# Performance work log

Hardware: AMD Instinct MI355X
Metric: run time of the kernel (lower is better)

The kernel has to match this reference:

```python
import jax, jax.numpy as jnp
import numpy as np

EMBED = 192
EXPAND = 3
D1 = EMBED * EXPAND  # 576
RPE_IN = 32
LAYERS = 3
LAMBDA = 0.95


def _rpe_mlp(t, w0, b0, ws, bs, wo, bo):
    # t: (2n, 1) relative positions -> (2n, D1) Toeplitz coefficients
    h = t @ w0.T + b0
    for i in range(ws.shape[0]):
        h = jax.nn.relu(h) @ ws[i].T + bs[i]
    return jax.nn.relu(h) @ wo.T + bo


def _toeplitz(x, a):
    # Toeplitz matmul via length-2n circular convolution (FFT).
    # x: (B, n, d); a: (2n, d) coeffs ordered [t0, t1..t_{n-1}, pad, neg half]
    n = x.shape[1]
    m = 2 * n
    xf = jnp.fft.rfft(x, m, axis=1)
    af = jnp.fft.rfft(a, m, axis=0)
    return jnp.fft.irfft(xf * af[None], m, axis=1)[:, :n]


def _forward(x, p_w, p_b, q_w, q_b, v_w, v_b, o_w, o_b, slope,
             t1_w0, t1_b0, t1_ws, t1_bs, t1_wo, t1_bo,
             t2_w0, t2_b0, t2_ws, t2_bs, t2_wo, t2_bo):
    b, h, w, d = x.shape
    n = h  # square grid: h == w, rpe/decay built from n = x.shape[1]
    dt = x.dtype

    pos = jnp.arange(1, n, dtype=dt).reshape(-1, 1)          # (n-1, 1)
    zero = jnp.zeros((1, 1), dt)
    rpe_input = jnp.concatenate([zero, pos, zero, -pos], axis=0)  # (2n, 1)

    p = jax.nn.silu(x @ p_w.T + p_b)
    q = jax.nn.silu(x @ q_w.T + q_b)
    v = jax.nn.silu(x @ v_w.T + v_b)

    # decay mask: slope clamped to [0,1], blended with lambda, powered by |lag|
    sl = LAMBDA + (1.0 - LAMBDA) * jnp.clip(slope, 0.0, 1.0)  # (1, D1)
    idx = jnp.arange(1, n, dtype=dt).reshape(1, -1, 1)        # (1, n-1, 1)
    gamma = sl ** idx                                          # (1, n-1, D1)
    one = jnp.ones((1, 1, D1), dt)
    decay = jnp.concatenate([one, gamma, one, gamma[:, ::-1]], axis=1)[0]  # (2n, D1)

    a1 = _rpe_mlp(rpe_input, t1_w0, t1_b0, t1_ws, t1_bs, t1_wo, t1_bo) * decay
    a2 = _rpe_mlp(rpe_input, t2_w0, t2_b0, t2_ws, t2_bs, t2_wo, t2_bo) * decay

    qv = q * v                                                 # (b, h, w, D1)
    # axial mixing: tno1 along width, tno2 along height
    o1 = _toeplitz(qv.reshape(b * h, w, D1), a1).reshape(b, h, w, D1)
    o2 = _toeplitz(jnp.transpose(qv, (0, 2, 1, 3)).reshape(b * w, h, D1), a2)
    o2 = jnp.transpose(o2.reshape(b, w, h, D1), (0, 2, 1, 3))
    out = p * (o1 + o2)
    return out @ o_w.T + o_b


def setup_inputs() -> dict:
    key = jax.random.key(0)
    ks = jax.random.split(key, 8)

    def lin(k, out_d, in_d):
        k1, k2 = jax.random.split(k)
        s = 1.0 / np.sqrt(in_d)
        return (jax.random.uniform(k1, (out_d, in_d), jnp.float32, -s, s),
                jax.random.uniform(k2, (out_d,), jnp.float32, -s, s))

    x = jax.random.normal(ks[0], (8, 56, 56, EMBED), jnp.float32)
    p_w, p_b = lin(ks[1], D1, EMBED)
    q_w, q_b = lin(ks[2], D1, EMBED)
    v_w, v_b = lin(ks[3], D1, EMBED)
    o_w, o_b = lin(ks[4], EMBED, D1)
    # slope init: 1/arange(1, d1+1)^(1/(index+1)), index=0
    slope = (1.0 / jnp.arange(1, D1 + 1, dtype=jnp.float32)).reshape(1, -1)

    def tno_params(kb):
        kk = jax.random.split(kb, 2 + LAYERS)
        w0, b0 = lin(kk[0], RPE_IN, 1)
        ws, bs = [], []
        for i in range(LAYERS):
            wi, bi = lin(kk[1 + i], RPE_IN, RPE_IN)
            ws.append(wi); bs.append(bi)
        wo, bo = lin(kk[1 + LAYERS], D1, RPE_IN)
        return w0, b0, jnp.stack(ws), jnp.stack(bs), wo, bo

    t1 = tno_params(ks[5])
    t2 = tno_params(ks[6])
    return {"x": x, "p_w": p_w, "p_b": p_b, "q_w": q_w, "q_b": q_b,
            "v_w": v_w, "v_b": v_b, "o_w": o_w, "o_b": o_b, "slope": slope,
            "t1_w0": t1[0], "t1_b0": t1[1], "t1_ws": t1[2], "t1_bs": t1[3], "t1_wo": t1[4], "t1_bo": t1[5],
            "t2_w0": t2[0], "t2_b0": t2[1], "t2_ws": t2[2], "t2_bs": t2[3], "t2_wo": t2[4], "t2_bo": t2[5]}


def reference(x, p_w, p_b, q_w, q_b, v_w, v_b, o_w, o_b, slope,
              t1_w0, t1_b0, t1_ws, t1_bs, t1_wo, t1_bo,
              t2_w0, t2_b0, t2_ws, t2_bs, t2_wo, t2_bo):
    return _forward(x, p_w, p_b, q_w, q_b, v_w, v_b, o_w, o_b, slope,
                    t1_w0, t1_b0, t1_ws, t1_bs, t1_wo, t1_bo,
                    t2_w0, t2_b0, t2_ws, t2_bs, t2_wo, t2_bo)
```

## Files before the change

### kernel.cpp

```cpp
#include <hip/hip_runtime.h>
#include <hip/hip_bf16.h>
#include <math.h>

typedef unsigned short u16;
typedef short bf16x8 __attribute__((ext_vector_type(8)));
typedef float f32x4 __attribute__((ext_vector_type(4)));

#define NB 8
#define NN 56
#define M2 112
#define EMB 192
#define D1 576
#define TOK (NB*NN*NN)

__device__ __forceinline__ float bf2f(unsigned int u) {
    union { unsigned int i; float f; } v; v.i = u << 16; return v.f;
}
__device__ __forceinline__ u16 f2bf(float f) {
    union { float f; unsigned int i; } v; v.f = f;
    unsigned int x = v.i;
    return (u16)((x + 0x7fffu + ((x >> 16) & 1u)) >> 16);
}
__device__ __forceinline__ float fast_silu(float x) {
    float e = __builtin_amdgcn_exp2f(-1.442695041f * x);
    return x * __builtin_amdgcn_rcpf(1.0f + e);
}
__device__ __forceinline__ void async16(void* lds, const void* g) {
    __builtin_amdgcn_global_load_lds(
        (const __attribute__((address_space(1))) void*)g,
        (__attribute__((address_space(3))) void*)lds, 16, 0, 0);
}

#define XCH (TOK*EMB/4)
#define WCH (D1*EMB/4)
__global__ __launch_bounds__(256) void convert_kernel(
    const float* __restrict__ x,
    const float* __restrict__ pw, const float* __restrict__ qw,
    const float* __restrict__ vw, const float* __restrict__ ow,
    u16* __restrict__ xb, u16* __restrict__ wb, u16* __restrict__ owb)
{
    int tid = blockIdx.x * 256 + threadIdx.x;
    const float* src; u16* dst; int off;
    if (tid < XCH) { src = x; dst = xb; off = tid; }
    else {
        int r = tid - XCH;
        int seg = r / WCH; off = r % WCH;
        if (seg == 0)      { src = pw; dst = wb; }
        else if (seg == 1) { src = qw; dst = wb + D1*EMB; }
        else if (seg == 2) { src = vw; dst = wb + 2*D1*EMB; }
        else if (seg == 3) { src = ow; dst = owb; }
        else return;
    }
    float4 f = *(const float4*)(src + off * 4);
    ushort4 o;
    o.x = f2bf(f.x); o.y = f2bf(f.y); o.z = f2bf(f.z); o.w = f2bf(f.w);
    *(ushort4*)(dst + off * 4) = o;
}

__global__ __launch_bounds__(576) void rpe_kernel(
    const float* __restrict__ slope,
    const float* w0a, const float* b0a, const float* wsa, const float* bsa,
    const float* woa, const float* boa,
    const float* w0b, const float* b0b, const float* wsb, const float* bsb,
    const float* wob, const float* bob,
    float* __restrict__ A1, float* __restrict__ A2)
{
    int wq  = blockIdx.x / M2;
    int row = blockIdx.x % M2;
    const float* w0 = wq ? w0b : w0a;  const float* b0 = wq ? b0b : b0a;
    const float* ws = wq ? wsb : wsa;  const float* bs = wq ? bsb : bsa;
    const float* wo = wq ? wob : woa;  const float* bo = wq ? bob : boa;
    float* A = wq ? A2 : A1;

    float tval = (row == 0 || row == 56) ? 0.0f
               : (row < 56 ? (float)row : -(float)(row - 56));
    int kexp = (row == 0 || row == 56) ? 0 : (row < 56 ? row : 112 - row);

    __shared__ float h[32], g[32];
    int t = threadIdx.x;
    if (t < 32) h[t] = tval * w0[t] + b0[t];
    __syncthreads();
    for (int L = 0; L < 3; L++) {
        if (t < 32) g[t] = fmaxf(h[t], 0.0f);
        __syncthreads();
        float hn = 0.0f;
        if (t < 32) {
            hn = bs[L * 32 + t];
            for (int k = 0; k < 32; k++)
                hn = fmaf(g[k], ws[(L * 32 + t) * 32 + k], hn);
        }
        __syncthreads();
        if (t < 32) h[t] = hn;
        __syncthreads();
    }
    if (t < 32) g[t] = fmaxf(h[t], 0.0f);
    __syncthreads();

    float o = bo[t];
    for (int k = 0; k < 32; k++)
        o = fmaf(g[k], wo[t * 32 + k], o);

    float sl = slope[t];
    sl = 0.95f + 0.05f * fminf(fmaxf(sl, 0.0f), 1.0f);
    float dec = powf(sl, (float)kexp);
    A[row * D1 + t] = o * dec;
}

__global__ __launch_bounds__(256) void tbuild_kernel(
    const float* __restrict__ A1, const float* __restrict__ A2,
    u16* __restrict__ T1t, u16* __restrict__ T2t)
{
    int d = blockIdx.x;
    const float* src = blockIdx.y ? A2 : A1;
    u16* dst = blockIdx.y ? T2t : T1t;
    __shared__ float win[111];
    int t = threadIdx.x;
    if (t < 111) {
        int lag = t - 55;
        int rowi = lag + (lag < 0 ? 112 : 0);
        win[t] = src[rowi * D1 + d];
    }
    __syncthreads();
    int i = t >> 2, jq = (t & 3) * 16;
    u16 vals[16];
    #pragma unroll
    for (int jj = 0; jj < 16; jj++) {
        int j = jq + jj;
        float v = (i < 56 && j < 56) ? win[i - j + 55] : 0.0f;
        vals[jj] = f2bf(v);
    }
    u16* out = dst + ((size_t)d * 64 + i) * 64 + jq;
    *(uint4*)(out)     = *(uint4*)&vals[0];
    *(uint4*)(out + 8) = *(uint4*)&vals[8];
}

__global__ __launch_bounds__(512, 4) void proj_kernel(
    const u16* __restrict__ xb, const u16* __restrict__ wb,
    const float* __restrict__ pb, const float* __restrict__ qb,
    const float* __restrict__ vb,
    u16* __restrict__ P_T, u16* __restrict__ QV_T)
{
    __shared__ u16 lds[20480];
    int m0 = blockIdx.x * 128, n0 = blockIdx.y * 64;
    int t = threadIdx.x;
    int l = t & 63, wave = t >> 6;
    int wm = wave >> 2, wn = wave & 3;
    int col16 = l & 15, q = l >> 4;

    f32x4 accp[4], accq[4], accv[4];
    #pragma unroll
    for (int i = 0; i < 4; i++) {
        accp[i] = (f32x4){0,0,0,0};
        accq[i] = (f32x4){0,0,0,0};
        accv[i] = (f32x4){0,0,0,0};
    }

    auto stage = [&](int kc) {
        #pragma unroll
        for (int ii = 0; ii < 2; ii++) {
            int slot = ii * 512 + t;
            int r = slot >> 3, s = slot & 7;
            int g = s ^ (r & 7);
            async16(&lds[slot * 8], xb + (m0 + r) * EMB + kc * 64 + g * 8);
        }
        #pragma unroll
        for (int ii = 0; ii < 3; ii++) {
            int slot = ii * 512 + t;
            int mat = slot >> 9, cc = slot & 511;
            int r = cc >> 3, s = cc & 7;
            int g = s ^ (r & 7);
            async16(&lds[8192 + slot * 8],
                    wb + mat * (D1 * EMB) + (n0 + r) * EMB + kc * 64 + g * 8);
        }
    };

    #pragma unroll
    for (int kc = 0; kc < 3; kc++) {
        stage(kc);
        asm volatile("s_waitcnt vmcnt(0)" ::: "memory");
        __builtin_amdgcn_s_barrier();
        #pragma unroll
        for (int kk = 0; kk < 2; kk++) {
            int sw = ((q + 4 * kk) ^ (col16 & 7)) * 8;
            bf16x8 af[4];
            #pragma unroll
            for (int mt = 0; mt < 4; mt++)
                af[mt] = *(const bf16x8*)&lds[(wm * 64 + mt * 16 + col16) * 64 + sw];
            bf16x8 bfr[3];
            #pragma unroll
            for (int mat = 0; mat < 3; mat++)
                bfr[mat] = *(const bf16x8*)&lds[8192 + mat * 4096 + (wn * 16 + col16) * 64 + sw];
            #pragma unroll
            for (int mt = 0; mt < 4; mt++) {
                accp[mt] = __builtin_amdgcn_mfma_f32_16x16x32_bf16(af[mt], bfr[0], accp[mt], 0, 0, 0);
                accq[mt] = __builtin_amdgcn_mfma_f32_16x16x32_bf16(af[mt], bfr[1], accq[mt], 0, 0, 0);
                accv[mt] = __builtin_amdgcn_mfma_f32_16x16x32_bf16(af[mt], bfr[2], accv[mt], 0, 0, 0);
            }
        }
        if (kc < 2) __builtin_amdgcn_s_barrier();
    }

    int n = n0 + wn * 16 + col16;
    float pbv = pb[n], qbv = qb[n], vbv = vb[n];
    size_t drow = (size_t)n * TOK + m0 + wm * 64;
    #pragma unroll
    for (int mt = 0; mt < 4; mt++) {
        ushort4 o;
        o.x = f2bf(fast_silu(accp[mt][0] + pbv));
        o.y = f2bf(fast_silu(accp[mt][1] + pbv));
        o.z = f2bf(fast_silu(accp[mt][2] + pbv));
        o.w = f2bf(fast_silu(accp[mt][3] + pbv));
        *(ushort4*)&P_T[drow + mt * 16 + q * 4] = o;
    }
    #pragma unroll
    for (int mt = 0; mt < 4; mt++) {
        ushort4 o;
        o.x = f2bf(fast_silu(accq[mt][0] + qbv) * fast_silu(accv[mt][0] + vbv));
        o.y = f2bf(fast_silu(accq[mt][1] + qbv) * fast_silu(accv[mt][1] + vbv));
        o.z = f2bf(fast_silu(accq[mt][2] + qbv) * fast_silu(accv[mt][2] + vbv));
        o.w = f2bf(fast_silu(accq[mt][3] + qbv) * fast_silu(accv[mt][3] + vbv));
        *(ushort4*)&QV_T[drow + mt * 16 + q * 4] = o;
    }
}

__global__ __launch_bounds__(256) void tno_mfma(
    const u16* __restrict__ QV_T, const u16* __restrict__ T1t,
    const u16* __restrict__ T2t, const u16* __restrict__ P_T,
    u16* __restrict__ U_T)
{
    __shared__ u16 T1s[4096];
    __shared__ u16 T2s[4096];
    __shared__ u16 Qn[64 * 72];
    __shared__ u16 Qt[64 * 72];
    __shared__ float O1f[56 * 68];
    int d = blockIdx.x, b = blockIdx.y;
    int t = threadIdx.x;
    size_t base = (size_t)d * TOK + (size_t)b * 3136;

    #pragma unroll
    for (int k = 0; k < 2; k++) {
        int slot = t + k * 256;
        int i = slot >> 3, s = slot & 7;
        int g = s ^ (i & 7);
        async16(&T1s[slot * 8], T1t + ((size_t)d * 64 + i) * 64 + g * 8);
        async16(&T2s[slot * 8], T2t + ((size_t)d * 64 + i) * 64 + g * 8);
    }
    for (int c = t; c < 392; c += 256) {
        int h = c / 7, w8 = (c % 7) * 8;
        uint4 v = *(const uint4*)(QV_T + base + c * 8);
        *(uint4*)&Qn[h * 72 + w8] = v;
        u16 e[8];
        *(uint4*)e = v;
        #pragma unroll
        for (int k = 0; k < 8; k++)
            Qt[(w8 + k) * 72 + h] = e[k];
    }
    if (t < 56) {
        uint4 z = {0, 0, 0, 0};
        *(uint4*)&Qn[t * 72 + 56] = z;
        *(uint4*)&Qt[t * 72 + 56] = z;
    }
    __syncthreads();

    int l = t & 63, wave = t >> 6;
    int col16 = l & 15, q = l >> 4;

    f32x4 acc1[4], acc2[4];
    #pragma unroll
    for (int i = 0; i < 4; i++) { acc1[i] = (f32x4){0,0,0,0}; acc2[i] = (f32x4){0,0,0,0}; }

    #pragma unroll
    for (int kk = 0; kk < 2; kk++) {
        int sw = ((q + 4 * kk) ^ (col16 & 7)) * 8;
        bf16x8 bq1 = *(const bf16x8*)&Qn[(wave * 16 + col16) * 72 + kk * 32 + q * 8];
        bf16x8 bq2 = *(const bf16x8*)&Qt[(wave * 16 + col16) * 72 + kk * 32 + q * 8];
        #pragma unroll
        for (int mt = 0; mt < 4; mt++) {
            bf16x8 a1 = *(const bf16x8*)&T1s[(mt * 16 + col16) * 64 + sw];
            bf16x8 a2 = *(const bf16x8*)&T2s[(mt * 16 + col16) * 64 + sw];
            acc1[mt] = __builtin_amdgcn_mfma_f32_16x16x32_bf16(a1, bq1, acc1[mt], 0, 0, 0);
            acc2[mt] = __builtin_amdgcn_mfma_f32_16x16x32_bf16(a2, bq2, acc2[mt], 0, 0, 0);
        }
    }

    {
        int n = wave * 16 + col16;
        if (n < 56) {
            #pragma unroll
            for (int mt = 0; mt < 4; mt++)
                #pragma unroll
                for (int r = 0; r < 4; r++) {
                    int m = mt * 16 + q * 4 + r;
                    if (m < 56) O1f[n * 68 + m] = acc1[mt][r];
                }
        }
    }
    __syncthreads();
    {
        int n = wave * 16 + col16;
        if (n < 56) {
            #pragma unroll
            for (int mt = 0; mt < 4; mt++)
                #pragma unroll
                for (int r = 0; r < 4; r++) {
                    int m = mt * 16 + q * 4 + r;
                    if (m < 56) O1f[m * 68 + n] += acc2[mt][r];
                }
        }
    }
    __syncthreads();
    for (int c = t; c < 392; c += 256) {
        int h = c / 7, w8 = (c % 7) * 8;
        f32x4 s0 = *(const f32x4*)&O1f[h * 68 + w8];
        f32x4 s1 = *(const f32x4*)&O1f[h * 68 + w8 + 4];
        uint4 pv = *(const uint4*)(P_T + base + c * 8);
        u16 pe[8];
        *(uint4*)pe = pv;
        u16 ue[8];
        #pragma unroll
        for (int k = 0; k < 4; k++) ue[k] = f2bf(bf2f(pe[k]) * s0[k]);
        #pragma unroll
        for (int k = 0; k < 4; k++) ue[4 + k] = f2bf(bf2f(pe[4 + k]) * s1[k]);
        *(uint4*)(U_T + base + c * 8) = *(uint4*)ue;
    }
}

__global__ __launch_bounds__(256) void outproj_kernel(
    const u16* __restrict__ U_T, const u16* __restrict__ owb,
    const float* __restrict__ ob, float* __restrict__ out)
{
    __shared__ char ldsraw[40960];
    u16* Uscr = (u16*)ldsraw;
    u16* As   = (u16*)(ldsraw + 16384);
    u16* Bs   = (u16*)(ldsraw + 32768);
    int m0 = blockIdx.x * 128, n0 = blockIdx.y * 64;
    int t = threadIdx.x;
    int l = t & 63, wave = t >> 6;
    int wm = wave >> 1, wn = wave & 1;
    int col16 = l & 15, q = l >> 4;

    f32x4 acc[4][2];
    #pragma unroll
    for (int i = 0; i < 4; i++)
        #pragma unroll
        for (int j = 0; j < 2; j++) acc[i][j] = (f32x4){0,0,0,0};

    for (int k0 = 0; k0 < 9; k0++) {
        #pragma unroll
        for (int ii = 0; ii < 4; ii++) {
            int slot = ii * 256 + t;
            int dd = slot >> 4, tk = slot & 15;
            async16(&Uscr[slot * 8],
                    U_T + (size_t)(k0 * 64 + dd) * TOK + m0 + tk * 8);
        }
        #pragma unroll
        for (int ii = 0; ii < 2; ii++) {
            int slot = ii * 256 + t;
            int r = slot >> 3, s = slot & 7;
            int g = s ^ (r & 7);
            async16(&Bs[slot * 8], owb + (n0 + r) * D1 + k0 * 64 + g * 8);
        }
        asm volatile("s_waitcnt vmcnt(2)" ::: "memory");
        __builtin_amdgcn_s_barrier();
        #pragma unroll
        for (int ii = 0; ii < 4; ii++) {
            int c = ii * 256 + t;
            int tok = c & 127, dc = c >> 7;
            u16 e[8];
            #pragma unroll
            for (int j = 0; j < 8; j++)
                e[j] = Uscr[(dc * 8 + j) * 128 + tok];
            int s = dc ^ (tok & 7);
            *(uint4*)&As[tok * 64 + s * 8] = *(uint4*)e;
        }
        __syncthreads();

        #pragma unroll
        for (int kk = 0; kk < 2; kk++) {
            int sw = ((q + 4 * kk) ^ (col16 & 7)) * 8;
            bf16x8 af[4];
            #pragma unroll
            for (int mt = 0; mt < 4; mt++)
                af[mt] = *(const bf16x8*)&As[(wm * 64 + mt * 16 + col16) * 64 + sw];
            bf16x8 bfr[2];
            #pragma unroll
            for (int nt = 0; nt < 2; nt++)
                bfr[nt] = *(const bf16x8*)&Bs[(wn * 32 + nt * 16 + col16) * 64 + sw];
            #pragma unroll
            for (int mt = 0; mt < 4; mt++)
                #pragma unroll
                for (int nt = 0; nt < 2; nt++)
                    acc[mt][nt] = __builtin_amdgcn_mfma_f32_16x16x32_bf16(
                        af[mt], bfr[nt], acc[mt][nt], 0, 0, 0);
        }
        __syncthreads();
    }

    float* scr = (float*)ldsraw + wave * 2304;
    float obv[2];
    #pragma unroll
    for (int nt = 0; nt < 2; nt++)
        obv[nt] = ob[n0 + wn * 32 + nt * 16 + col16];
    #pragma unroll
    for (int mt = 0; mt < 4; mt++)
        #pragma unroll
        for (int nt = 0; nt < 2; nt++)
            #pragma unroll
            for (int r = 0; r < 4; r++)
                scr[(mt * 16 + q * 4 + r) * 36 + nt * 16 + col16] =
                    acc[mt][nt][r] + obv[nt];
    __syncthreads();
    #pragma unroll
    for (int k = 0; k < 8; k++) {
        int row = k * 8 + (l >> 3), cs = (l & 7) * 4;
        f32x4 v = *(const f32x4*)&scr[row * 36 + cs];
        *(f32x4*)&out[(m0 + wm * 64 + row) * EMB + n0 + wn * 32 + cs] = v;
    }
}

extern "C" void kernel_launch(void* const* d_in, const int* in_sizes, int n_in,
                              void* d_out, int out_size, void* d_ws, size_t ws_size,
                              hipStream_t stream)
{
    (void)in_sizes; (void)n_in; (void)out_size; (void)ws_size;
    const float* x     = (const float*)d_in[0];
    const float* p_w   = (const float*)d_in[1];
    const float* p_b   = (const float*)d_in[2];
    const float* q_w   = (const float*)d_in[3];
    const float* q_b   = (const float*)d_in[4];
    const float* v_w   = (const float*)d_in[5];
    const float* v_b   = (const float*)d_in[6];
    const float* o_w   = (const float*)d_in[7];
    const float* o_b   = (const float*)d_in[8];
    const float* slope = (const float*)d_in[9];
    const float* t1_w0 = (const float*)d_in[10];
    const float* t1_b0 = (const float*)d_in[11];
    const float* t1_ws = (const float*)d_in[12];
    const float* t1_bs = (const float*)d_in[13];
    const float* t1_wo = (const float*)d_in[14];
    const float* t1_bo = (const float*)d_in[15];
    const float* t2_w0 = (const float*)d_in[16];
    const float* t2_b0 = (const float*)d_in[17];
    const float* t2_ws = (const float*)d_in[18];
    const float* t2_bs = (const float*)d_in[19];
    const float* t2_wo = (const float*)d_in[20];
    const float* t2_bo = (const float*)d_in[21];

    char* ws = (char*)d_ws;
    float* A1  = (float*)ws;
    float* A2  = (float*)(ws + 258048);
    u16*   PT  = (u16*)(ws + 516096);
    u16*   QVT = (u16*)(ws + 29417472);
    u16*   UT  = (u16*)(ws + 58318848);
    u16*   xb  = (u16*)(ws + 87220224);
    u16*   wb  = (u16*)(ws + 96854016);
    u16*   owb = (u16*)(ws + 97517568);
    u16*   T1t = (u16*)(ws + 97738752);
    u16*   T2t = (u16*)(ws + 102457344);

    convert_kernel<<<(XCH + 4*WCH + 255) / 256, 256, 0, stream>>>(
        x, p_w, q_w, v_w, o_w, xb, wb, owb);
    rpe_kernel<<<224, 576, 0, stream>>>(slope,
        t1_w0, t1_b0, t1_ws, t1_bs, t1_wo, t1_bo,
        t2_w0, t2_b0, t2_ws, t2_bs, t2_wo, t2_bo, A1, A2);
    tbuild_kernel<<<dim3(576, 2), 256, 0, stream>>>(A1, A2, T1t, T2t);
    proj_kernel<<<dim3(TOK / 128, D1 / 64), 512, 0, stream>>>(
        xb, wb, p_b, q_b, v_b, PT, QVT);
    tno_mfma<<<dim3(D1, NB), 256, 0, stream>>>(QVT, T1t, T2t, PT, UT);
    outproj_kernel<<<dim3(TOK / 128, EMB / 64), 256, 0, stream>>>(
        UT, owb, o_b, (float*)d_out);
}
```

Measured before the change: 203.7 us.

## Fuse convert, RPE and Toeplitz build; double-buffer outproj; prefetch P in TNO

Merges the bf16 conversion, the RPE MLP and the Toeplitz-matrix build into one prep kernel, so two launches and the A1/A2 round trip through global memory go away. Each Toeplitz block now recomputes the small MLP for all 112 rows itself. The output-projection GEMM gets double-buffered async loads with explicit waitcnt/barrier control, which grows LDS to 64KB and may reduce occupancy. The TNO kernel also loads its P values at the start so that latency overlaps the MFMA work.

Measured after the change: 259.5 us. 27.4% more time.

```diff
diff --git a/kernel.cpp b/kernel.cpp
--- a/kernel.cpp
+++ b/kernel.cpp
@@ -33,94 +33,96 @@
 
 #define XCH (TOK*EMB/4)
 #define WCH (D1*EMB/4)
-__global__ __launch_bounds__(256) void convert_kernel(
+#define CONVB ((XCH + 4*WCH) / 256)
+__global__ __launch_bounds__(256) void prep_kernel(
     const float* __restrict__ x,
     const float* __restrict__ pw, const float* __restrict__ qw,
     const float* __restrict__ vw, const float* __restrict__ ow,
-    u16* __restrict__ xb, u16* __restrict__ wb, u16* __restrict__ owb)
+    u16* __restrict__ xb, u16* __restrict__ wb, u16* __restrict__ owb,
+    const float* __restrict__ slope,
+    const float* __restrict__ w0a, const float* __restrict__ b0a,
+    const float* __restrict__ wsa, const float* __restrict__ bsa,
+    const float* __restrict__ woa, const float* __restrict__ boa,
+    const float* __restrict__ w0b, const float* __restrict__ b0b,
+    const float* __restrict__ wsb, const float* __restrict__ bsb,
+    const float* __restrict__ wob, const float* __restrict__ bob,
+    u16* __restrict__ T1t, u16* __restrict__ T2t)
 {
-    int tid = blockIdx.x * 256 + threadIdx.x;
-    const float* src; u16* dst; int off;
-    if (tid < XCH) { src = x; dst = xb; off = tid; }
-    else {
-        int r = tid - XCH;
-        int seg = r / WCH; off = r % WCH;
-        if (seg == 0)      { src = pw; dst = wb; }
-        else if (seg == 1) { src = qw; dst = wb + D1*EMB; }
-        else if (seg == 2) { src = vw; dst = wb + 2*D1*EMB; }
-        else if (seg == 3) { src = ow; dst = owb; }
-        else return;
-    }
-    float4 f = *(const float4*)(src + off * 4);
-    ushort4 o;
-    o.x = f2bf(f.x); o.y = f2bf(f.y); o.z = f2bf(f.z); o.w = f2bf(f.w);
-    *(ushort4*)(dst + off * 4) = o;
-}
-
-__global__ __launch_bounds__(576) void rpe_kernel(
-    const float* __restrict__ slope,
-    const float* w0a, const float* b0a, const float* wsa, const float* bsa,
-    const float* woa, const float* boa,
-    const float* w0b, const float* b0b, const float* wsb, const float* bsb,
-    const float* wob, const float* bob,
-    float* __restrict__ A1, float* __restrict__ A2)
-{
-    int wq  = blockIdx.x / M2;
-    int row = blockIdx.x % M2;
+    int t = threadIdx.x;
+    if (blockIdx.x < CONVB) {
+        int tid = blockIdx.x * 256 + t;
+        const float* src; u16* dst; int off;
+        if (tid < XCH) { src = x; dst = xb; off = tid; }
+        else {
+            int r = tid - XCH;
+            int seg = r / WCH; off = r % WCH;
+            if (seg == 0)      { src = pw; dst = wb; }
+            else if (seg == 1) { src = qw; dst = wb + D1*EMB; }
+            else if (seg == 2) { src = vw; dst = wb + 2*D1*EMB; }
+            else               { src = ow; dst = owb; }
+        }
+        float4 f = *(const float4*)(src + off * 4);
+        ushort4 o;
+        o.x = f2bf(f.x); o.y = f2bf(f.y); o.z = f2bf(f.z); o.w = f2bf(f.w);
+        *(ushort4*)(dst + off * 4) = o;
+        return;
+    }
+
+    int idx = blockIdx.x - CONVB;
+    int d  = idx % D1;
+    int wq = idx / D1;
     const float* w0 = wq ? w0b : w0a;  const float* b0 = wq ? b0b : b0a;
     const float* ws = wq ? wsb : wsa;  const float* bs = wq ? bsb : bsa;
     const float* wo = wq ? wob : woa;  const float* bo = wq ? bob : boa;
-    float* A = wq ? A2 : A1;
-
-    float tval = (row == 0 || row == 56) ? 0.0f
-               : (row < 56 ? (float)row : -(float)(row - 56));
-    int kexp = (row == 0 || row == 56) ? 0 : (row < 56 ? row : 112 - row);
-
-    __shared__ float h[32], g[32];
-    int t = threadIdx.x;
-    if (t < 32) h[t] = tval * w0[t] + b0[t];
-    __syncthreads();
-    for (int L = 0; L < 3; L++) {
-        if (t < 32) g[t] = fmaxf(h[t], 0.0f);
-        __syncthreads();
-        float hn = 0.0f;
-        if (t < 32) {
-            hn = bs[L * 32 + t];
+    u16* dst = wq ? T2t : T1t;
+
+    __shared__ float wss[3][32][32];
+    __shared__ float gbuf[112][33];
+    __shared__ float hbuf[8][33];
+    __shared__ float win[128];
+
+    for (int i = t; i < 3072; i += 256) {
+        int L = i >> 10, r = (i >> 5) & 31, k = i & 31;
+        wss[L][k][r] = ws[(L * 32 + r) * 32 + k];
+    }
+    __syncthreads();
+
+    int rg = t >> 5, lane = t & 31;
+    float w0v = w0[lane], b0v = b0[lane];
+    float bsv0 = bs[lane], bsv1 = bs[32 + lane], bsv2 = bs[64 + lane];
+    for (int base = 0; base < 112; base += 8) {
+        int row = base + rg;
+        float tval = (row == 0 || row == 56) ? 0.0f
+                   : (row < 56 ? (float)row : -(float)(row - 56));
+        float h = tval * w0v + b0v;
+        #pragma unroll
+        for (int L = 0; L < 3; L++) {
+            hbuf[rg][lane] = h;
+            __syncthreads();
+            float hn = (L == 0) ? bsv0 : (L == 1) ? bsv1 : bsv2;
+            #pragma unroll
             for (int k = 0; k < 32; k++)
-                hn = fmaf(g[k], ws[(L * 32 + t) * 32 + k], hn);
-        }
-        __syncthreads();
-        if (t < 32) h[t] = hn;
-        __syncthreads();
-    }
-    if (t < 32) g[t] = fmaxf(h[t], 0.0f);
-    __syncthreads();
-
-    float o = bo[t];
-    for (int k = 0; k < 32; k++)
-        o = fmaf(g[k], wo[t * 32 + k], o);
-
-    float sl = slope[t];
-    sl = 0.95f + 0.05f * fminf(fmaxf(sl, 0.0f), 1.0f);
-    float dec = powf(sl, (float)kexp);
-    A[row * D1 + t] = o * dec;
-}
-
-__global__ __launch_bounds__(256) void tbuild_kernel(
-    const float* __restrict__ A1, const float* __restrict__ A2,
-    u16* __restrict__ T1t, u16* __restrict__ T2t)
-{
-    int d = blockIdx.x;
-    const float* src = blockIdx.y ? A2 : A1;
-    u16* dst = blockIdx.y ? T2t : T1t;
-    __shared__ float win[111];
-    int t = threadIdx.x;
+                hn = fmaf(fmaxf(hbuf[rg][k], 0.0f), wss[L][k][lane], hn);
+            __syncthreads();
+            h = hn;
+        }
+        gbuf[row][lane] = fmaxf(h, 0.0f);
+    }
+    __syncthreads();
+
+    float sl = 0.95f + 0.05f * fminf(fmaxf(slope[d], 0.0f), 1.0f);
     if (t < 111) {
         int lag = t - 55;
         int rowi = lag + (lag < 0 ? 112 : 0);
-        win[t] = src[rowi * D1 + d];
-    }
-    __syncthreads();
+        float o = bo[d];
+        #pragma unroll
+        for (int k = 0; k < 32; k++)
+            o = fmaf(gbuf[rowi][k], wo[d * 32 + k], o);
+        int kexp = (rowi == 0 || rowi == 56) ? 0 : (rowi < 56 ? rowi : 112 - rowi);
+        win[t] = o * powf(sl, (float)kexp);
+    }
+    __syncthreads();
+
     int i = t >> 2, jq = (t & 3) * 16;
     u16 vals[16];
     #pragma unroll
@@ -237,6 +239,11 @@
     int t = threadIdx.x;
     size_t base = (size_t)d * TOK + (size_t)b * 3136;
 
+    uint4 pv0 = *(const uint4*)(P_T + base + t * 8);
+    uint4 pv1 = {0,0,0,0};
+    bool has2 = (t + 256) < 392;
+    if (has2) pv1 = *(const uint4*)(P_T + base + (t + 256) * 8);
+
     #pragma unroll
     for (int k = 0; k < 2; k++) {
         int slot = t + k * 256;
@@ -309,13 +316,27 @@
         }
     }
     __syncthreads();
-    for (int c = t; c < 392; c += 256) {
+    {
+        int c = t;
         int h = c / 7, w8 = (c % 7) * 8;
         f32x4 s0 = *(const f32x4*)&O1f[h * 68 + w8];
         f32x4 s1 = *(const f32x4*)&O1f[h * 68 + w8 + 4];
-        uint4 pv = *(const uint4*)(P_T + base + c * 8);
         u16 pe[8];
-        *(uint4*)pe = pv;
+        *(uint4*)pe = pv0;
+        u16 ue[8];
+        #pragma unroll
+        for (int k = 0; k < 4; k++) ue[k] = f2bf(bf2f(pe[k]) * s0[k]);
+        #pragma unroll
+        for (int k = 0; k < 4; k++) ue[4 + k] = f2bf(bf2f(pe[4 + k]) * s1[k]);
+        *(uint4*)(U_T + base + c * 8) = *(uint4*)ue;
+    }
+    if (has2) {
+        int c = t + 256;
+        int h = c / 7, w8 = (c % 7) * 8;
+        f32x4 s0 = *(const f32x4*)&O1f[h * 68 + w8];
+        f32x4 s1 = *(const f32x4*)&O1f[h * 68 + w8 + 4];
+        u16 pe[8];
+        *(uint4*)pe = pv1;
         u16 ue[8];
         #pragma unroll
         for (int k = 0; k < 4; k++) ue[k] = f2bf(bf2f(pe[k]) * s0[k]);
@@ -329,10 +350,10 @@
     const u16* __restrict__ U_T, const u16* __restrict__ owb,
     const float* __restrict__ ob, float* __restrict__ out)
 {
-    __shared__ char ldsraw[40960];
+    __shared__ char ldsraw[65536];
     u16* Uscr = (u16*)ldsraw;
-    u16* As   = (u16*)(ldsraw + 16384);
-    u16* Bs   = (u16*)(ldsraw + 32768);
+    u16* As   = (u16*)(ldsraw + 32768);
+    u16* Bs   = (u16*)(ldsraw + 49152);
     int m0 = blockIdx.x * 128, n0 = blockIdx.y * 64;
     int t = threadIdx.x;
     int l = t & 63, wave = t >> 6;
@@ -345,12 +366,14 @@
         #pragma unroll
         for (int j = 0; j < 2; j++) acc[i][j] = (f32x4){0,0,0,0};
 
-    for (int k0 = 0; k0 < 9; k0++) {
+    auto stage = [&](int k0, int buf) {
+        u16* Us = Uscr + buf * 8192;
+        u16* Bss = Bs + buf * 4096;
         #pragma unroll
         for (int ii = 0; ii < 4; ii++) {
             int slot = ii * 256 + t;
             int dd = slot >> 4, tk = slot & 15;
-            async16(&Uscr[slot * 8],
+            async16(&Us[slot * 8],
                     U_T + (size_t)(k0 * 64 + dd) * TOK + m0 + tk * 8);
         }
         #pragma unroll
@@ -358,10 +381,21 @@
             int slot = ii * 256 + t;
             int r = slot >> 3, s = slot & 7;
             int g = s ^ (r & 7);
-            async16(&Bs[slot * 8], owb + (n0 + r) * D1 + k0 * 64 + g * 8);
-        }
-        asm volatile("s_waitcnt vmcnt(2)" ::: "memory");
+            async16(&Bss[slot * 8], owb + (n0 + r) * D1 + k0 * 64 + g * 8);
+        }
+    };
+
+    stage(0, 0);
+    for (int k0 = 0; k0 < 9; k0++) {
+        int buf = k0 & 1;
+        if (k0 < 8) {
+            stage(k0 + 1, buf ^ 1);
+            asm volatile("s_waitcnt vmcnt(6)" ::: "memory");
+        } else {
+            asm volatile("s_waitcnt vmcnt(0)" ::: "memory");
+        }
         __builtin_amdgcn_s_barrier();
+        u16* Us = Uscr + buf * 8192;
         #pragma unroll
         for (int ii = 0; ii < 4; ii++) {
             int c = ii * 256 + t;
@@ -369,12 +403,14 @@
             u16 e[8];
             #pragma unroll
             for (int j = 0; j < 8; j++)
-                e[j] = Uscr[(dc * 8 + j) * 128 + tok];
+                e[j] = Us[(dc * 8 + j) * 128 + tok];
             int s = dc ^ (tok & 7);
             *(uint4*)&As[tok * 64 + s * 8] = *(uint4*)e;
         }
-        __syncthreads();
-
+        asm volatile("s_waitcnt lgkmcnt(0)" ::: "memory");
+        __builtin_amdgcn_s_barrier();
+
+        u16* Bss = Bs + buf * 4096;
         #pragma unroll
         for (int kk = 0; kk < 2; kk++) {
             int sw = ((q + 4 * kk) ^ (col16 & 7)) * 8;
@@ -385,7 +421,7 @@
             bf16x8 bfr[2];
             #pragma unroll
             for (int nt = 0; nt < 2; nt++)
-                bfr[nt] = *(const bf16x8*)&Bs[(wn * 32 + nt * 16 + col16) * 64 + sw];
+                bfr[nt] = *(const bf16x8*)&Bss[(wn * 32 + nt * 16 + col16) * 64 + sw];
             #pragma unroll
             for (int mt = 0; mt < 4; mt++)
                 #pragma unroll
@@ -393,7 +429,8 @@
                     acc[mt][nt] = __builtin_amdgcn_mfma_f32_16x16x32_bf16(
                         af[mt], bfr[nt], acc[mt][nt], 0, 0, 0);
         }
-        __syncthreads();
+        asm volatile("s_waitcnt lgkmcnt(0)" ::: "memory");
+        __builtin_amdgcn_s_barrier();
     }
 
     float* scr = (float*)ldsraw + wave * 2304;
@@ -447,8 +484,6 @@
     const float* t2_bo = (const float*)d_in[21];
 
     char* ws = (char*)d_ws;
-    float* A1  = (float*)ws;
-    float* A2  = (float*)(ws + 258048);
     u16*   PT  = (u16*)(ws + 516096);
     u16*   QVT = (u16*)(ws + 29417472);
     u16*   UT  = (u16*)(ws + 58318848);
@@ -458,12 +493,10 @@
     u16*   T1t = (u16*)(ws + 97738752);
     u16*   T2t = (u16*)(ws + 102457344);
 
-    convert_kernel<<<(XCH + 4*WCH + 255) / 256, 256, 0, stream>>>(
-        x, p_w, q_w, v_w, o_w, xb, wb, owb);
-    rpe_kernel<<<224, 576, 0, stream>>>(slope,
+    prep_kernel<<<CONVB + 2 * D1, 256, 0, stream>>>(
+        x, p_w, q_w, v_w, o_w, xb, wb, owb, slope,
         t1_w0, t1_b0, t1_ws, t1_bs, t1_wo, t1_bo,
-        t2_w0, t2_b0, t2_ws, t2_bs, t2_wo, t2_bo, A1, A2);
-    tbuild_kernel<<<dim3(576, 2), 256, 0, stream>>>(A1, A2, T1t, T2t);
+        t2_w0, t2_b0, t2_ws, t2_bs, t2_wo, t2_bo, T1t, T2t);
     proj_kernel<<<dim3(TOK / 128, D1 / 64), 512, 0, stream>>>(
         xb, wb, p_b, q_b, v_b, PT, QVT);
     tno_mfma<<<dim3(D1, NB), 256, 0, stream>>>(QVT, T1t, T2t, PT, UT);
```
